# Performance work log

Hardware: AMD Instinct MI355X
Metric: run time of the kernel (lower is better)

## Reference

```python
import jax, jax.numpy as jnp
import numpy as np

DIM = 1024
HID = 2 * DIM
NUM_EXPERTS = 8
TOP_K = 2
BATCH, SEQ = 2, 2048


def setup_inputs() -> dict:
    key = jax.random.key(0)
    ks = jax.random.split(key, 8)
    s = 0.02
    return {
        "x": jax.random.normal(ks[0], (BATCH, SEQ, DIM), jnp.float32),
        "router_w": jax.random.normal(ks[1], (DIM, NUM_EXPERTS), jnp.float32) * s,
        "router_b": jnp.zeros((NUM_EXPERTS,), jnp.float32),
        "sw1": jax.random.normal(ks[2], (DIM, HID), jnp.float32) * s,
        "sb1": jnp.zeros((HID,), jnp.float32),
        "sw2": jax.random.normal(ks[3], (HID, DIM), jnp.float32) * s,
        "sb2": jnp.zeros((DIM,), jnp.float32),
        "ew1": jax.random.normal(ks[4], (NUM_EXPERTS, DIM, HID), jnp.float32) * s,
        "eb1": jnp.zeros((NUM_EXPERTS, HID), jnp.float32),
        "ew2": jax.random.normal(ks[5], (NUM_EXPERTS, HID, DIM), jnp.float32) * s,
        "eb2": jnp.zeros((NUM_EXPERTS, DIM), jnp.float32),
    }


def _gelu(x):
    # torch nn.GELU default is the exact (erf) form
    return jax.nn.gelu(x, approximate=False)


def reference(x, router_w, router_b, sw1, sb1, sw2, sb2, ew1, eb1, ew2, eb2):
    B, S, D = x.shape
    flat = x.reshape(-1, D)                      # [T, D]
    T = flat.shape[0]

    # Router: softmax -> top-k -> renormalize
    probs = jax.nn.softmax(flat @ router_w + router_b, axis=-1)  # [T, E]
    top_w, top_i = jax.lax.top_k(probs, TOP_K)                   # [T, K]
    top_w = top_w / jnp.sum(top_w, axis=-1, keepdims=True)
    # Dense per-token combine weights [T, E] (zero for unrouted experts)
    comb = jnp.zeros_like(probs).at[jnp.arange(T)[:, None], top_i].set(top_w)

    # Shared expert (always on)
    shared = _gelu(flat @ sw1 + sb1) @ sw2 + sb2                 # [T, D]

    # All experts as one batched GEMM pair; zero weights kill unrouted tokens.
    h = _gelu(jnp.einsum('td,edh->eth', flat, ew1) + eb1[:, None, :])  # [E, T, H]
    eo = jnp.einsum('eth,ehd->etd', h, ew2) + eb2[:, None, :]          # [E, T, D]
    moe = jnp.einsum('te,etd->td', comb, eo)                           # [T, D]

    return (shared + moe).reshape(B, S, D)
```

## Files before the change

### kernel.cpp

```cpp
#include <hip/hip_runtime.h>

#define DIM   1024
#define HID   2048
#define NE    8
#define T_TOK 4096

typedef __attribute__((ext_vector_type(8))) short short8;
typedef __attribute__((ext_vector_type(4))) float f32x4;

__device__ __forceinline__ ushort f2bf(float f) {
    union { float f; unsigned u; } v; v.f = f;
    unsigned r = v.u + 0x7FFFu + ((v.u >> 16) & 1u);
    return (ushort)(r >> 16);
}

__device__ __forceinline__ float gelu_fast(float x) {
    float t = x * x;
    float u = x * (1.0f + 0.044715f * t);
    float e = exp2f(2.3020585f * u);
    return x - x / (e + 1.0f);
}

__global__ void transpose_conv9(const float* __restrict__ ew, const float* __restrict__ sw,
                                ushort* __restrict__ ewT, ushort* __restrict__ swT,
                                int R, int C) {
    __shared__ float tile[32][65];
    int z = blockIdx.z;
    const float* in = (z < NE) ? ew + (size_t)z * R * C : sw;
    ushort* out     = (z < NE) ? ewT + (size_t)z * R * C : swT;
    int c0 = blockIdx.x * 32, r0 = blockIdx.y * 64;
    int tx = threadIdx.x & 31, ty = threadIdx.x >> 5;
#pragma unroll
    for (int rr = 0; rr < 64; rr += 8)
        tile[tx][rr + ty] = in[(size_t)(r0 + rr + ty) * C + (c0 + tx)];
    __syncthreads();
    int lane = threadIdx.x & 63, q = threadIdx.x >> 6;
#pragma unroll
    for (int j = 0; j < 8; ++j) {
        int cc = q * 8 + j;
        out[(size_t)(c0 + cc) * R + (r0 + lane)] = f2bf(tile[cc][lane]);
    }
}

__global__ void router_kernel(const float* __restrict__ x, const float* __restrict__ rw,
                              const float* __restrict__ rb, int* __restrict__ cnt,
                              int* __restrict__ ids, float* __restrict__ wts,
                              int* __restrict__ te, int* __restrict__ tp,
                              ushort* __restrict__ xb) {
    int wave = threadIdx.x >> 6;
    int lane = threadIdx.x & 63;
    int t = blockIdx.x * 4 + wave;
    const float* xr = x + (size_t)t * DIM;
    ushort* xo = xb + (size_t)t * DIM;
    float acc[NE];
#pragma unroll
    for (int e = 0; e < NE; ++e) acc[e] = 0.f;
    {
        int d0 = lane * 16;
        float v[16];
#pragma unroll
        for (int j = 0; j < 16; j += 4) {
            float4 f = *(const float4*)(xr + d0 + j);
            v[j] = f.x; v[j+1] = f.y; v[j+2] = f.z; v[j+3] = f.w;
        }
        short8 o0, o1;
#pragma unroll
        for (int j = 0; j < 8; ++j) { o0[j] = (short)f2bf(v[j]); o1[j] = (short)f2bf(v[8+j]); }
        *(short8*)(xo + d0)     = o0;
        *(short8*)(xo + d0 + 8) = o1;
#pragma unroll
        for (int j = 0; j < 16; ++j) {
#pragma unroll
            for (int e = 0; e < NE; ++e) acc[e] += v[j] * rw[(d0 + j) * NE + e];
        }
    }
#pragma unroll
    for (int e = 0; e < NE; ++e) {
#pragma unroll
        for (int off = 32; off; off >>= 1) acc[e] += __shfl_xor(acc[e], off);
    }
    if (lane == 0) {
        float l[NE];
#pragma unroll
        for (int e = 0; e < NE; ++e) l[e] = acc[e] + rb[e];
        int i1 = 0;
#pragma unroll
        for (int e = 1; e < NE; ++e) if (l[e] > l[i1]) i1 = e;
        int i2 = (i1 == 0) ? 1 : 0;
#pragma unroll
        for (int e = 0; e < NE; ++e) if (e != i1 && l[e] > l[i2]) i2 = e;
        float p2 = __expf(l[i2] - l[i1]);
        float w1 = 1.0f / (1.0f + p2);
        float w2 = p2 / (1.0f + p2);
        int pos1 = atomicAdd(&cnt[i1], 1);
        ids[i1 * T_TOK + pos1] = t; wts[i1 * T_TOK + pos1] = w1;
        te[2 * t] = i1; tp[2 * t] = pos1;
        int pos2 = atomicAdd(&cnt[i2], 1);
        ids[i2 * T_TOK + pos2] = t; wts[i2 * T_TOK + pos2] = w2;
        te[2 * t + 1] = i2; tp[2 * t + 1] = pos2;
    }
}

__global__ void build_queue(const int* __restrict__ cnt, int* __restrict__ offs,
                            int* __restrict__ q1, int* __restrict__ n1,
                            int* __restrict__ q2, int* __restrict__ n2) {
    if (threadIdx.x != 0) return;
    int s = 0;
    for (int e = 0; e < NE; ++e) { offs[e] = s; s += cnt[e]; }
    int k1 = 0, k2 = 0;
    for (int z = 0; z <= NE; ++z) {
        int c = (z < NE) ? cnt[z] : T_TOK;
        int mts = (c + 255) >> 8;
        for (int mt = 0; mt < mts; ++mt) {
            for (int nt = 0; nt < HID / 256; ++nt)
                q1[k1++] = (z << 16) | (mt << 8) | nt;
            for (int nt = 0; nt < DIM / 256; ++nt)
                q2[k2++] = (z << 16) | (mt << 8) | nt;
        }
    }
    *n1 = k1; *n2 = k2;
}

__device__ __forceinline__ void mma256(
    const ushort* __restrict__ A, const int* __restrict__ gather, int count,
    const ushort* __restrict__ BT, int K, int tileM, int tileN,
    ushort* lds, f32x4 acc[8][4])
{
    const int tid  = threadIdx.x;
    const int lane = tid & 63, wave = tid >> 6;
    const int wr = wave >> 2, wc = wave & 3;
    const int g = lane >> 4, fr = lane & 15;
    const int swl = (fr & 7) << 3;
    const int sub = lane >> 3;
    const int kcs = ((lane & 7) ^ sub) << 3;

    const ushort* asrc[4];
    const ushort* bsrc[4];
#pragma unroll
    for (int i = 0; i < 4; ++i) {
        int row = (wave * 4 + i) * 8 + sub;
        int ar = tileM + row; if (ar > count - 1) ar = count - 1;
        int grow = gather ? gather[ar] : ar;
        asrc[i] = A  + (size_t)grow * K + kcs;
        bsrc[i] = BT + (size_t)(tileN + row) * K + kcs;
    }

    auto STAGE = [&](int buf, int t) {
        ushort* base = lds + buf * 32768;
#pragma unroll
        for (int i = 0; i < 4; ++i) {
            int chunk = wave * 4 + i;
            __builtin_amdgcn_global_load_lds(
                (const __attribute__((address_space(1))) void*)(asrc[i] + t * 64),
                (__attribute__((address_space(3))) void*)(base + chunk * 512),
                16, 0, 0);
            __builtin_amdgcn_global_load_lds(
                (const __attribute__((address_space(1))) void*)(bsrc[i] + t * 64),
                (__attribute__((address_space(3))) void*)(base + 16384 + chunk * 512),
                16, 0, 0);
        }
    };

    auto COMPUTE = [&](int buf) {
        const ushort* A_s = lds + buf * 32768;
        const ushort* B_s = A_s + 16384;
#pragma unroll
        for (int kk = 0; kk < 2; ++kk) {
            int koff = (kk * 32 + g * 8) ^ swl;
            short8 a[8], b[4];
#pragma unroll
            for (int m = 0; m < 8; ++m) {
                int row = wr * 128 + m * 16 + fr;
                a[m] = *(const short8*)&A_s[row * 64 + koff];
            }
#pragma unroll
            for (int n = 0; n < 4; ++n) {
                int col = wc * 64 + n * 16 + fr;
                b[n] = *(const short8*)&B_s[col * 64 + koff];
            }
#pragma unroll
            for (int m = 0; m < 8; ++m)
#pragma unroll
                for (int n = 0; n < 4; ++n)
                    acc[m][n] = __builtin_amdgcn_mfma_f32_16x16x32_bf16(
                        a[m], b[n], acc[m][n], 0, 0, 0);
        }
    };

    const int NT = K >> 6;
    STAGE(0, 0);
    for (int t = 0; t < NT; ++t) {
        int cur = t & 1;
        if (t + 1 < NT) {
            STAGE(cur ^ 1, t + 1);
            asm volatile("s_waitcnt vmcnt(8)" ::: "memory");
        } else {
            asm volatile("s_waitcnt vmcnt(0)" ::: "memory");
        }
        __builtin_amdgcn_s_barrier();
        asm volatile("" ::: "memory");
        COMPUTE(cur);
        asm volatile("" ::: "memory");
        __builtin_amdgcn_s_barrier();
    }
}

__global__ __launch_bounds__(512, 2)
void gemm1_kernel(const ushort* __restrict__ xb,
                  const ushort* __restrict__ ew1T, const ushort* __restrict__ sw1T,
                  const float* __restrict__ eb1, const float* __restrict__ sb1,
                  const int* __restrict__ ids, const int* __restrict__ cnt,
                  const int* __restrict__ offs,
                  const int* __restrict__ q1, const int* __restrict__ n1,
                  ushort* __restrict__ h)
{
    extern __shared__ ushort lds[];
    const int nit = *n1;
    const int lane = threadIdx.x & 63, wave = threadIdx.x >> 6;
    const int wr = wave >> 2, wc = wave & 3, g = lane >> 4, fr = lane & 15;

    for (int it = blockIdx.x; it < nit; it += gridDim.x) {
        int item = q1[it];
        int z = item >> 16, mt = (item >> 8) & 255, nt = item & 255;
        int count, hbase;
        const ushort* BT; const float* bias; const int* gather;
        if (z < NE) {
            count  = cnt[z];
            BT     = ew1T + (size_t)z * HID * DIM;
            bias   = eb1 + z * HID;
            gather = ids + z * T_TOK;
            hbase  = T_TOK + offs[z];
        } else {
            count = T_TOK; BT = sw1T; bias = sb1; gather = nullptr; hbase = 0;
        }
        int tileM = mt * 256, tileN = nt * 256;

        f32x4 acc[8][4];
#pragma unroll
        for (int m = 0; m < 8; ++m)
#pragma unroll
            for (int n = 0; n < 4; ++n) acc[m][n] = (f32x4){0.f, 0.f, 0.f, 0.f};

        mma256(xb, gather, count, BT, DIM, tileM, tileN, lds, acc);

#pragma unroll
        for (int n = 0; n < 4; ++n) {
            int col = tileN + wc * 64 + n * 16 + fr;
            float bc = bias[col];
#pragma unroll
            for (int m = 0; m < 8; ++m) {
#pragma unroll
                for (int i = 0; i < 4; ++i) {
                    int row = tileM + wr * 128 + m * 16 + g * 4 + i;
                    if (row < count)
                        h[(size_t)(hbase + row) * HID + col] =
                            f2bf(gelu_fast(acc[m][n][i] + bc));
                }
            }
        }
        __syncthreads();
    }
}

__global__ __launch_bounds__(512, 2)
void gemm2_kernel(const ushort* __restrict__ h,
                  const ushort* __restrict__ ew2T, const ushort* __restrict__ sw2T,
                  const float* __restrict__ eb2, const float* __restrict__ sb2,
                  const float* __restrict__ wts,
                  const int* __restrict__ cnt, const int* __restrict__ offs,
                  const int* __restrict__ q2, const int* __restrict__ n2,
                  float* __restrict__ eo, float* __restrict__ out)
{
    extern __shared__ ushort lds[];
    const int nit = *n2;
    const int lane = threadIdx.x & 63, wave = threadIdx.x >> 6;
    const int wr = wave >> 2, wc = wave & 3, g = lane >> 4, fr = lane & 15;

    for (int it = blockIdx.x; it < nit; it += gridDim.x) {
        int item = q2[it];
        int z = item >> 16, mt = (item >> 8) & 255, nt = item & 255;
        int count;
        const ushort* BT; const float* bias; const float* tw; float* dst;
        const ushort* Arows;
        if (z < NE) {
            count = cnt[z];
            BT    = ew2T + (size_t)z * DIM * HID;
            bias  = eb2 + z * DIM;
            tw    = wts + z * T_TOK;
            Arows = h + (size_t)(T_TOK + offs[z]) * HID;
            dst   = eo + (size_t)offs[z] * DIM;
        } else {
            count = T_TOK; BT = sw2T; bias = sb2; tw = nullptr;
            Arows = h;
            dst   = out;
        }
        int tileM = mt * 256, tileN = nt * 256;

        f32x4 acc[8][4];
#pragma unroll
        for (int m = 0; m < 8; ++m)
#pragma unroll
            for (int n = 0; n < 4; ++n) acc[m][n] = (f32x4){0.f, 0.f, 0.f, 0.f};

        mma256(Arows, nullptr, count, BT, HID, tileM, tileN, lds, acc);

#pragma unroll
        for (int m = 0; m < 8; ++m) {
#pragma unroll
            for (int i = 0; i < 4; ++i) {
                int row = tileM + wr * 128 + m * 16 + g * 4 + i;
                if (row < count) {
                    float w = tw ? tw[row] : 1.0f;
#pragma unroll
                    for (int n = 0; n < 4; ++n) {
                        int col = tileN + wc * 64 + n * 16 + fr;
                        dst[(size_t)row * DIM + col] = w * (acc[m][n][i] + bias[col]);
                    }
                }
            }
        }
        __syncthreads();
    }
}

__global__ void combine_kernel(const float* __restrict__ eo, const int* __restrict__ te,
                               const int* __restrict__ tp, const int* __restrict__ offs,
                               float* __restrict__ out)
{
    int t = blockIdx.x;
    int s1 = offs[te[2 * t]]     + tp[2 * t];
    int s2 = offs[te[2 * t + 1]] + tp[2 * t + 1];
    int d = threadIdx.x * 4;
    float4 a = *(const float4*)(out + (size_t)t * DIM + d);
    float4 b = *(const float4*)(eo + (size_t)s1 * DIM + d);
    float4 c = *(const float4*)(eo + (size_t)s2 * DIM + d);
    a.x += b.x + c.x; a.y += b.y + c.y; a.z += b.z + c.z; a.w += b.w + c.w;
    *(float4*)(out + (size_t)t * DIM + d) = a;
}

extern "C" void kernel_launch(void* const* d_in, const int* in_sizes, int n_in,
                              void* d_out, int out_size, void* d_ws, size_t ws_size,
                              hipStream_t stream)
{
    const float* x   = (const float*)d_in[0];
    const float* rw  = (const float*)d_in[1];
    const float* rb  = (const float*)d_in[2];
    const float* sw1 = (const float*)d_in[3];
    const float* sb1 = (const float*)d_in[4];
    const float* sw2 = (const float*)d_in[5];
    const float* sb2 = (const float*)d_in[6];
    const float* ew1 = (const float*)d_in[7];
    const float* eb1 = (const float*)d_in[8];
    const float* ew2 = (const float*)d_in[9];
    const float* eb2 = (const float*)d_in[10];
    float* out = (float*)d_out;

    char* p = (char*)d_ws;
    ushort* xb   = (ushort*)p;  p += (size_t)T_TOK * DIM * 2;
    ushort* sw1T = (ushort*)p;  p += (size_t)HID * DIM * 2;
    ushort* sw2T = (ushort*)p;  p += (size_t)DIM * HID * 2;
    ushort* ew1T = (ushort*)p;  p += (size_t)NE * HID * DIM * 2;
    ushort* ew2T = (ushort*)p;  p += (size_t)NE * DIM * HID * 2;
    ushort* hbuf = (ushort*)p;  p += (size_t)(3 * T_TOK) * HID * 2;
    float*  eo   = (float*)p;   p += (size_t)(2 * T_TOK) * DIM * 4;
    int*    ids  = (int*)p;     p += (size_t)NE * T_TOK * 4;
    float*  wts  = (float*)p;   p += (size_t)NE * T_TOK * 4;
    int*    te   = (int*)p;     p += (size_t)2 * T_TOK * 4;
    int*    tp   = (int*)p;     p += (size_t)2 * T_TOK * 4;
    int*    cnt  = (int*)p;     p += 256;
    int*    offs = (int*)p;     p += 256;
    int*    q1   = (int*)p;     p += 4608;
    int*    q2   = (int*)p;     p += 2304;
    int*    nq   = (int*)p;     p += 256;

    hipFuncSetAttribute((const void*)gemm1_kernel,
                        hipFuncAttributeMaxDynamicSharedMemorySize, 131072);
    hipFuncSetAttribute((const void*)gemm2_kernel,
                        hipFuncAttributeMaxDynamicSharedMemorySize, 131072);

    hipMemsetAsync(cnt, 0, 256, stream);

    router_kernel<<<dim3(T_TOK / 4), 256, 0, stream>>>(x, rw, rb, cnt, ids, wts, te, tp, xb);
    transpose_conv9<<<dim3(HID / 32, DIM / 64, NE + 1), 256, 0, stream>>>(
        ew1, sw1, ew1T, sw1T, DIM, HID);
    transpose_conv9<<<dim3(DIM / 32, HID / 64, NE + 1), 256, 0, stream>>>(
        ew2, sw2, ew2T, sw2T, HID, DIM);
    build_queue<<<dim3(1), 64, 0, stream>>>(cnt, offs, q1, nq, q2, nq + 1);
    gemm1_kernel<<<dim3(256), 512, 131072, stream>>>(
        xb, ew1T, sw1T, eb1, sb1, ids, cnt, offs, q1, nq, hbuf);
    gemm2_kernel<<<dim3(256), 512, 131072, stream>>>(
        hbuf, ew2T, sw2T, eb2, sb2, wts, cnt, offs, q2, nq + 1, eo, out);
    combine_kernel<<<dim3(T_TOK), 256, 0, stream>>>(eo, te, tp, offs, out);
}
```

Measured before the change: 348.4 us.

## Shrink GEMM tiles to 128x128 with atomic work queue and single-buffered LDS

Both grouped GEMMs move from 256x256 tiles with 512 threads and a double-buffered 128KB LDS pipeline to 128x128 tiles with 256 threads, a single 32KB static LDS buffer and plain __syncthreads between load and compute. Work items are now claimed dynamically through an atomic counter instead of a static grid-stride loop, with 1024 blocks launched. The intent is finer load balancing across the uneven per-expert tiles and higher occupancy. In exchange it lowers arithmetic intensity per tile and drops the overlap of global loads with MFMA compute.

New measurement: 368.1 us. 1.06x slower.

```diff
diff --git a/kernel.cpp b/kernel.cpp
--- a/kernel.cpp
+++ b/kernel.cpp
@@ -102,37 +102,38 @@
 }
 
 __global__ void build_queue(const int* __restrict__ cnt, int* __restrict__ offs,
-                            int* __restrict__ q1, int* __restrict__ n1,
-                            int* __restrict__ q2, int* __restrict__ n2) {
+                            int* __restrict__ q1, int* __restrict__ q2,
+                            int* __restrict__ nq) {
     if (threadIdx.x != 0) return;
     int s = 0;
     for (int e = 0; e < NE; ++e) { offs[e] = s; s += cnt[e]; }
     int k1 = 0, k2 = 0;
     for (int z = 0; z <= NE; ++z) {
         int c = (z < NE) ? cnt[z] : T_TOK;
-        int mts = (c + 255) >> 8;
+        int mts = (c + 127) >> 7;
         for (int mt = 0; mt < mts; ++mt) {
-            for (int nt = 0; nt < HID / 256; ++nt)
+            for (int nt = 0; nt < HID / 128; ++nt)
                 q1[k1++] = (z << 16) | (mt << 8) | nt;
-            for (int nt = 0; nt < DIM / 256; ++nt)
+            for (int nt = 0; nt < DIM / 128; ++nt)
                 q2[k2++] = (z << 16) | (mt << 8) | nt;
         }
     }
-    *n1 = k1; *n2 = k2;
-}
-
-__device__ __forceinline__ void mma256(
+    nq[0] = k1; nq[1] = k2;
+    nq[2] = 0;  nq[3] = 0;
+}
+
+__device__ __forceinline__ void mma_tile(
     const ushort* __restrict__ A, const int* __restrict__ gather, int count,
     const ushort* __restrict__ BT, int K, int tileM, int tileN,
-    ushort* lds, f32x4 acc[8][4])
+    ushort* lds, f32x4 acc[4][4])
 {
     const int tid  = threadIdx.x;
     const int lane = tid & 63, wave = tid >> 6;
-    const int wr = wave >> 2, wc = wave & 3;
     const int g = lane >> 4, fr = lane & 15;
     const int swl = (fr & 7) << 3;
     const int sub = lane >> 3;
     const int kcs = ((lane & 7) ^ sub) << 3;
+    const int wr = wave >> 1, wc = wave & 1;
 
     const ushort* asrc[4];
     const ushort* bsrc[4];
@@ -145,81 +146,66 @@
         bsrc[i] = BT + (size_t)(tileN + row) * K + kcs;
     }
 
-    auto STAGE = [&](int buf, int t) {
-        ushort* base = lds + buf * 32768;
+    const int NT = K >> 6;
+    for (int t = 0; t < NT; ++t) {
 #pragma unroll
         for (int i = 0; i < 4; ++i) {
             int chunk = wave * 4 + i;
             __builtin_amdgcn_global_load_lds(
                 (const __attribute__((address_space(1))) void*)(asrc[i] + t * 64),
-                (__attribute__((address_space(3))) void*)(base + chunk * 512),
+                (__attribute__((address_space(3))) void*)(lds + chunk * 512),
                 16, 0, 0);
             __builtin_amdgcn_global_load_lds(
                 (const __attribute__((address_space(1))) void*)(bsrc[i] + t * 64),
-                (__attribute__((address_space(3))) void*)(base + 16384 + chunk * 512),
+                (__attribute__((address_space(3))) void*)(lds + 8192 + chunk * 512),
                 16, 0, 0);
         }
-    };
-
-    auto COMPUTE = [&](int buf) {
-        const ushort* A_s = lds + buf * 32768;
-        const ushort* B_s = A_s + 16384;
+        __syncthreads();
 #pragma unroll
         for (int kk = 0; kk < 2; ++kk) {
             int koff = (kk * 32 + g * 8) ^ swl;
-            short8 a[8], b[4];
-#pragma unroll
-            for (int m = 0; m < 8; ++m) {
-                int row = wr * 128 + m * 16 + fr;
-                a[m] = *(const short8*)&A_s[row * 64 + koff];
+            short8 a[4], b[4];
+#pragma unroll
+            for (int m = 0; m < 4; ++m) {
+                int row = wr * 64 + m * 16 + fr;
+                a[m] = *(const short8*)&lds[row * 64 + koff];
             }
 #pragma unroll
             for (int n = 0; n < 4; ++n) {
                 int col = wc * 64 + n * 16 + fr;
-                b[n] = *(const short8*)&B_s[col * 64 + koff];
+                b[n] = *(const short8*)&lds[8192 + col * 64 + koff];
             }
 #pragma unroll
-            for (int m = 0; m < 8; ++m)
+            for (int m = 0; m < 4; ++m)
 #pragma unroll
                 for (int n = 0; n < 4; ++n)
                     acc[m][n] = __builtin_amdgcn_mfma_f32_16x16x32_bf16(
                         a[m], b[n], acc[m][n], 0, 0, 0);
         }
-    };
-
-    const int NT = K >> 6;
-    STAGE(0, 0);
-    for (int t = 0; t < NT; ++t) {
-        int cur = t & 1;
-        if (t + 1 < NT) {
-            STAGE(cur ^ 1, t + 1);
-            asm volatile("s_waitcnt vmcnt(8)" ::: "memory");
-        } else {
-            asm volatile("s_waitcnt vmcnt(0)" ::: "memory");
-        }
-        __builtin_amdgcn_s_barrier();
-        asm volatile("" ::: "memory");
-        COMPUTE(cur);
-        asm volatile("" ::: "memory");
-        __builtin_amdgcn_s_barrier();
-    }
-}
-
-__global__ __launch_bounds__(512, 2)
+        __syncthreads();
+    }
+}
+
+__global__ __launch_bounds__(256, 4)
 void gemm1_kernel(const ushort* __restrict__ xb,
                   const ushort* __restrict__ ew1T, const ushort* __restrict__ sw1T,
                   const float* __restrict__ eb1, const float* __restrict__ sb1,
                   const int* __restrict__ ids, const int* __restrict__ cnt,
                   const int* __restrict__ offs,
-                  const int* __restrict__ q1, const int* __restrict__ n1,
-                  ushort* __restrict__ h)
-{
-    extern __shared__ ushort lds[];
-    const int nit = *n1;
+                  const int* __restrict__ q1, const int* __restrict__ nq,
+                  int* __restrict__ qc, ushort* __restrict__ h)
+{
+    __shared__ ushort lds[16384];
+    __shared__ int s_it;
+    const int nit = nq[0];
     const int lane = threadIdx.x & 63, wave = threadIdx.x >> 6;
-    const int wr = wave >> 2, wc = wave & 3, g = lane >> 4, fr = lane & 15;
-
-    for (int it = blockIdx.x; it < nit; it += gridDim.x) {
+    const int wr = wave >> 1, wc = wave & 1, g = lane >> 4, fr = lane & 15;
+
+    for (;;) {
+        if (threadIdx.x == 0) s_it = atomicAdd(qc, 1);
+        __syncthreads();
+        int it = s_it;
+        if (it >= nit) break;
         int item = q1[it];
         int z = item >> 16, mt = (item >> 8) & 255, nt = item & 255;
         int count, hbase;
@@ -233,50 +219,54 @@
         } else {
             count = T_TOK; BT = sw1T; bias = sb1; gather = nullptr; hbase = 0;
         }
-        int tileM = mt * 256, tileN = nt * 256;
-
-        f32x4 acc[8][4];
-#pragma unroll
-        for (int m = 0; m < 8; ++m)
+        int tileM = mt * 128, tileN = nt * 128;
+
+        f32x4 acc[4][4];
+#pragma unroll
+        for (int m = 0; m < 4; ++m)
 #pragma unroll
             for (int n = 0; n < 4; ++n) acc[m][n] = (f32x4){0.f, 0.f, 0.f, 0.f};
 
-        mma256(xb, gather, count, BT, DIM, tileM, tileN, lds, acc);
+        mma_tile(xb, gather, count, BT, DIM, tileM, tileN, lds, acc);
 
 #pragma unroll
         for (int n = 0; n < 4; ++n) {
             int col = tileN + wc * 64 + n * 16 + fr;
             float bc = bias[col];
 #pragma unroll
-            for (int m = 0; m < 8; ++m) {
+            for (int m = 0; m < 4; ++m) {
 #pragma unroll
                 for (int i = 0; i < 4; ++i) {
-                    int row = tileM + wr * 128 + m * 16 + g * 4 + i;
+                    int row = tileM + wr * 64 + m * 16 + g * 4 + i;
                     if (row < count)
                         h[(size_t)(hbase + row) * HID + col] =
                             f2bf(gelu_fast(acc[m][n][i] + bc));
                 }
             }
         }
-        __syncthreads();
-    }
-}
-
-__global__ __launch_bounds__(512, 2)
+    }
+}
+
+__global__ __launch_bounds__(256, 4)
 void gemm2_kernel(const ushort* __restrict__ h,
                   const ushort* __restrict__ ew2T, const ushort* __restrict__ sw2T,
                   const float* __restrict__ eb2, const float* __restrict__ sb2,
                   const float* __restrict__ wts,
                   const int* __restrict__ cnt, const int* __restrict__ offs,
-                  const int* __restrict__ q2, const int* __restrict__ n2,
-                  float* __restrict__ eo, float* __restrict__ out)
-{
-    extern __shared__ ushort lds[];
-    const int nit = *n2;
+                  const int* __restrict__ q2, const int* __restrict__ nq,
+                  int* __restrict__ qc, float* __restrict__ eo, float* __restrict__ out)
+{
+    __shared__ ushort lds[16384];
+    __shared__ int s_it;
+    const int nit = nq[1];
     const int lane = threadIdx.x & 63, wave = threadIdx.x >> 6;
-    const int wr = wave >> 2, wc = wave & 3, g = lane >> 4, fr = lane & 15;
-
-    for (int it = blockIdx.x; it < nit; it += gridDim.x) {
+    const int wr = wave >> 1, wc = wave & 1, g = lane >> 4, fr = lane & 15;
+
+    for (;;) {
+        if (threadIdx.x == 0) s_it = atomicAdd(qc, 1);
+        __syncthreads();
+        int it = s_it;
+        if (it >= nit) break;
         int item = q2[it];
         int z = item >> 16, mt = (item >> 8) & 255, nt = item & 255;
         int count;
@@ -294,21 +284,21 @@
             Arows = h;
             dst   = out;
         }
-        int tileM = mt * 256, tileN = nt * 256;
-
-        f32x4 acc[8][4];
-#pragma unroll
-        for (int m = 0; m < 8; ++m)
+        int tileM = mt * 128, tileN = nt * 128;
+
+        f32x4 acc[4][4];
+#pragma unroll
+        for (int m = 0; m < 4; ++m)
 #pragma unroll
             for (int n = 0; n < 4; ++n) acc[m][n] = (f32x4){0.f, 0.f, 0.f, 0.f};
 
-        mma256(Arows, nullptr, count, BT, HID, tileM, tileN, lds, acc);
-
-#pragma unroll
-        for (int m = 0; m < 8; ++m) {
+        mma_tile(Arows, nullptr, count, BT, HID, tileM, tileN, lds, acc);
+
+#pragma unroll
+        for (int m = 0; m < 4; ++m) {
 #pragma unroll
             for (int i = 0; i < 4; ++i) {
-                int row = tileM + wr * 128 + m * 16 + g * 4 + i;
+                int row = tileM + wr * 64 + m * 16 + g * 4 + i;
                 if (row < count) {
                     float w = tw ? tw[row] : 1.0f;
 #pragma unroll
@@ -319,7 +309,6 @@
                 }
             }
         }
-        __syncthreads();
     }
 }
 
@@ -369,14 +358,9 @@
     int*    tp   = (int*)p;     p += (size_t)2 * T_TOK * 4;
     int*    cnt  = (int*)p;     p += 256;
     int*    offs = (int*)p;     p += 256;
-    int*    q1   = (int*)p;     p += 4608;
-    int*    q2   = (int*)p;     p += 2304;
+    int*    q1   = (int*)p;     p += 16384;
+    int*    q2   = (int*)p;     p += 8192;
     int*    nq   = (int*)p;     p += 256;
-
-    hipFuncSetAttribute((const void*)gemm1_kernel,
-                        hipFuncAttributeMaxDynamicSharedMemorySize, 131072);
-    hipFuncSetAttribute((const void*)gemm2_kernel,
-                        hipFuncAttributeMaxDynamicSharedMemorySize, 131072);
 
     hipMemsetAsync(cnt, 0, 256, stream);
 
@@ -385,10 +369,10 @@
         ew1, sw1, ew1T, sw1T, DIM, HID);
     transpose_conv9<<<dim3(DIM / 32, HID / 64, NE + 1), 256, 0, stream>>>(
         ew2, sw2, ew2T, sw2T, HID, DIM);
-    build_queue<<<dim3(1), 64, 0, stream>>>(cnt, offs, q1, nq, q2, nq + 1);
-    gemm1_kernel<<<dim3(256), 512, 131072, stream>>>(
-        xb, ew1T, sw1T, eb1, sb1, ids, cnt, offs, q1, nq, hbuf);
-    gemm2_kernel<<<dim3(256), 512, 131072, stream>>>(
-        hbuf, ew2T, sw2T, eb2, sb2, wts, cnt, offs, q2, nq + 1, eo, out);
+    build_queue<<<dim3(1), 64, 0, stream>>>(cnt, offs, q1, q2, nq);
+    gemm1_kernel<<<dim3(1024), 256, 0, stream>>>(
+        xb, ew1T, sw1T, eb1, sb1, ids, cnt, offs, q1, nq, nq + 2, hbuf);
+    gemm2_kernel<<<dim3(1024), 256, 0, stream>>>(
+        hbuf, ew2T, sw2T, eb2, sb2, wts, cnt, offs, q2, nq, nq + 3, eo, out);
     combine_kernel<<<dim3(T_TOK), 256, 0, stream>>>(eo, te, tp, offs, out);
 }
```

## Use 128x128 tiles with atomic work queue in gemm1, 4 waves per block

Applied to the files above, without the earlier changes.

Replaces gemm1's 256x256 double-buffered tile loop with a 128x128 single-buffered tile on 256-thread blocks using 32KB static LDS, so more blocks fit per CU. Work items are now fetched through an atomic counter rather than a fixed grid-stride loop, which lets blocks balance the uneven per-expert tile counts dynamically. The smaller tiles give finer granularity and better tail balance, at the cost of lower data reuse per tile. The loss of double buffering also exposes global-to-LDS latency on every K step.

Result: no change. 352.5 us (+1.2%).

```diff
diff --git a/kernel.cpp b/kernel.cpp
--- a/kernel.cpp
+++ b/kernel.cpp
@@ -102,23 +102,89 @@
 }
 
 __global__ void build_queue(const int* __restrict__ cnt, int* __restrict__ offs,
-                            int* __restrict__ q1, int* __restrict__ n1,
-                            int* __restrict__ q2, int* __restrict__ n2) {
+                            int* __restrict__ q1, int* __restrict__ q2,
+                            int* __restrict__ nq) {
     if (threadIdx.x != 0) return;
     int s = 0;
     for (int e = 0; e < NE; ++e) { offs[e] = s; s += cnt[e]; }
     int k1 = 0, k2 = 0;
     for (int z = 0; z <= NE; ++z) {
         int c = (z < NE) ? cnt[z] : T_TOK;
-        int mts = (c + 255) >> 8;
-        for (int mt = 0; mt < mts; ++mt) {
-            for (int nt = 0; nt < HID / 256; ++nt)
+        int mts1 = (c + 127) >> 7;
+        for (int mt = 0; mt < mts1; ++mt)
+            for (int nt = 0; nt < HID / 128; ++nt)
                 q1[k1++] = (z << 16) | (mt << 8) | nt;
+        int mts2 = (c + 255) >> 8;
+        for (int mt = 0; mt < mts2; ++mt)
             for (int nt = 0; nt < DIM / 256; ++nt)
                 q2[k2++] = (z << 16) | (mt << 8) | nt;
-        }
-    }
-    *n1 = k1; *n2 = k2;
+    }
+    nq[0] = k1; nq[1] = k2;
+    nq[2] = 0;  nq[3] = 0;
+}
+
+__device__ __forceinline__ void mma_tile(
+    const ushort* __restrict__ A, const int* __restrict__ gather, int count,
+    const ushort* __restrict__ BT, int K, int tileM, int tileN,
+    ushort* lds, f32x4 acc[4][4])
+{
+    const int tid  = threadIdx.x;
+    const int lane = tid & 63, wave = tid >> 6;
+    const int g = lane >> 4, fr = lane & 15;
+    const int swl = (fr & 7) << 3;
+    const int sub = lane >> 3;
+    const int kcs = ((lane & 7) ^ sub) << 3;
+    const int wr = wave >> 1, wc = wave & 1;
+
+    const ushort* asrc[4];
+    const ushort* bsrc[4];
+#pragma unroll
+    for (int i = 0; i < 4; ++i) {
+        int row = (wave * 4 + i) * 8 + sub;
+        int ar = tileM + row; if (ar > count - 1) ar = count - 1;
+        int grow = gather ? gather[ar] : ar;
+        asrc[i] = A  + (size_t)grow * K + kcs;
+        bsrc[i] = BT + (size_t)(tileN + row) * K + kcs;
+    }
+
+    const int NT = K >> 6;
+    for (int t = 0; t < NT; ++t) {
+#pragma unroll
+        for (int i = 0; i < 4; ++i) {
+            int chunk = wave * 4 + i;
+            __builtin_amdgcn_global_load_lds(
+                (const __attribute__((address_space(1))) void*)(asrc[i] + t * 64),
+                (__attribute__((address_space(3))) void*)(lds + chunk * 512),
+                16, 0, 0);
+            __builtin_amdgcn_global_load_lds(
+                (const __attribute__((address_space(1))) void*)(bsrc[i] + t * 64),
+                (__attribute__((address_space(3))) void*)(lds + 8192 + chunk * 512),
+                16, 0, 0);
+        }
+        __syncthreads();
+#pragma unroll
+        for (int kk = 0; kk < 2; ++kk) {
+            int koff = (kk * 32 + g * 8) ^ swl;
+            short8 a[4], b[4];
+#pragma unroll
+            for (int m = 0; m < 4; ++m) {
+                int row = wr * 64 + m * 16 + fr;
+                a[m] = *(const short8*)&lds[row * 64 + koff];
+            }
+#pragma unroll
+            for (int n = 0; n < 4; ++n) {
+                int col = wc * 64 + n * 16 + fr;
+                b[n] = *(const short8*)&lds[8192 + col * 64 + koff];
+            }
+#pragma unroll
+            for (int m = 0; m < 4; ++m)
+#pragma unroll
+                for (int n = 0; n < 4; ++n)
+                    acc[m][n] = __builtin_amdgcn_mfma_f32_16x16x32_bf16(
+                        a[m], b[n], acc[m][n], 0, 0, 0);
+        }
+        __syncthreads();
+    }
 }
 
 __device__ __forceinline__ void mma256(
@@ -205,21 +271,26 @@
     }
 }
 
-__global__ __launch_bounds__(512, 2)
+__global__ __launch_bounds__(256, 4)
 void gemm1_kernel(const ushort* __restrict__ xb,
                   const ushort* __restrict__ ew1T, const ushort* __restrict__ sw1T,
                   const float* __restrict__ eb1, const float* __restrict__ sb1,
                   const int* __restrict__ ids, const int* __restrict__ cnt,
                   const int* __restrict__ offs,
-                  const int* __restrict__ q1, const int* __restrict__ n1,
-                  ushort* __restrict__ h)
-{
-    extern __shared__ ushort lds[];
-    const int nit = *n1;
+                  const int* __restrict__ q1, const int* __restrict__ nq,
+                  int* __restrict__ qc, ushort* __restrict__ h)
+{
+    __shared__ ushort lds[16384];
+    __shared__ int s_it;
+    const int nit = nq[0];
     const int lane = threadIdx.x & 63, wave = threadIdx.x >> 6;
-    const int wr = wave >> 2, wc = wave & 3, g = lane >> 4, fr = lane & 15;
-
-    for (int it = blockIdx.x; it < nit; it += gridDim.x) {
+    const int wr = wave >> 1, wc = wave & 1, g = lane >> 4, fr = lane & 15;
+
+    for (;;) {
+        if (threadIdx.x == 0) s_it = atomicAdd(qc, 1);
+        __syncthreads();
+        int it = s_it;
+        if (it >= nit) break;
         int item = q1[it];
         int z = item >> 16, mt = (item >> 8) & 255, nt = item & 255;
         int count, hbase;
@@ -233,32 +304,31 @@
         } else {
             count = T_TOK; BT = sw1T; bias = sb1; gather = nullptr; hbase = 0;
         }
-        int tileM = mt * 256, tileN = nt * 256;
-
-        f32x4 acc[8][4];
-#pragma unroll
-        for (int m = 0; m < 8; ++m)
+        int tileM = mt * 128, tileN = nt * 128;
+
+        f32x4 acc[4][4];
+#pragma unroll
+        for (int m = 0; m < 4; ++m)
 #pragma unroll
             for (int n = 0; n < 4; ++n) acc[m][n] = (f32x4){0.f, 0.f, 0.f, 0.f};
 
-        mma256(xb, gather, count, BT, DIM, tileM, tileN, lds, acc);
+        mma_tile(xb, gather, count, BT, DIM, tileM, tileN, lds, acc);
 
 #pragma unroll
         for (int n = 0; n < 4; ++n) {
             int col = tileN + wc * 64 + n * 16 + fr;
             float bc = bias[col];
 #pragma unroll
-            for (int m = 0; m < 8; ++m) {
+            for (int m = 0; m < 4; ++m) {
 #pragma unroll
                 for (int i = 0; i < 4; ++i) {
-                    int row = tileM + wr * 128 + m * 16 + g * 4 + i;
+                    int row = tileM + wr * 64 + m * 16 + g * 4 + i;
                     if (row < count)
                         h[(size_t)(hbase + row) * HID + col] =
                             f2bf(gelu_fast(acc[m][n][i] + bc));
                 }
             }
         }
-        __syncthreads();
     }
 }
 
@@ -369,12 +439,10 @@
     int*    tp   = (int*)p;     p += (size_t)2 * T_TOK * 4;
     int*    cnt  = (int*)p;     p += 256;
     int*    offs = (int*)p;     p += 256;
-    int*    q1   = (int*)p;     p += 4608;
-    int*    q2   = (int*)p;     p += 2304;
+    int*    q1   = (int*)p;     p += 16384;
+    int*    q2   = (int*)p;     p += 8192;
     int*    nq   = (int*)p;     p += 256;
 
-    hipFuncSetAttribute((const void*)gemm1_kernel,
-                        hipFuncAttributeMaxDynamicSharedMemorySize, 131072);
     hipFuncSetAttribute((const void*)gemm2_kernel,
                         hipFuncAttributeMaxDynamicSharedMemorySize, 131072);
 
@@ -385,9 +453,9 @@
         ew1, sw1, ew1T, sw1T, DIM, HID);
     transpose_conv9<<<dim3(DIM / 32, HID / 64, NE + 1), 256, 0, stream>>>(
         ew2, sw2, ew2T, sw2T, HID, DIM);
-    build_queue<<<dim3(1), 64, 0, stream>>>(cnt, offs, q1, nq, q2, nq + 1);
-    gemm1_kernel<<<dim3(256), 512, 131072, stream>>>(
-        xb, ew1T, sw1T, eb1, sb1, ids, cnt, offs, q1, nq, hbuf);
+    build_queue<<<dim3(1), 64, 0, stream>>>(cnt, offs, q1, q2, nq);
+    gemm1_kernel<<<dim3(1024), 256, 0, stream>>>(
+        xb, ew1T, sw1T, eb1, sb1, ids, cnt, offs, q1, nq, nq + 2, hbuf);
     gemm2_kernel<<<dim3(256), 512, 131072, stream>>>(
         hbuf, ew2T, sw2T, eb2, sb2, wts, cnt, offs, q2, nq + 1, eo, out);
     combine_kernel<<<dim3(T_TOK), 256, 0, stream>>>(eo, te, tp, offs, out);
```
